# Kernel optimization log

Hardware: AMD Instinct MI355X
Metric: run time of the kernel (lower is better)

The kernel has to match this reference:

```python
import jax, jax.numpy as jnp
import numpy as np

H, C = 8, 16            # heads, per-head channels (at_channels)
HID = H * C             # 128
N_NODES = 50000
N_EDGES = 400000
N_GRAPHS = 500
SPEC = 1000


def setup_inputs() -> dict:
    key = jax.random.key(0)
    ks = jax.random.split(key, 32)
    s = 0.05

    def rn(k, shape):
        return jax.random.normal(k, shape, jnp.float32) * s

    inp = {}
    inp["x"] = jax.random.normal(ks[0], (N_NODES, 16), jnp.float32)
    inp["edge_index"] = jax.random.randint(ks[1], (2, N_EDGES), 0, N_NODES, jnp.int32)
    inp["edge_attr"] = jax.random.normal(ks[2], (N_EDGES, 2), jnp.float32)
    inp["batch"] = jnp.sort(jax.random.randint(ks[3], (N_NODES,), 0, N_GRAPHS, jnp.int32))
    # layer 1 (input dim 16)
    inp["at1_Wl"] = rn(ks[4], (16, HID)); inp["at1_bl"] = rn(ks[5], (HID,))
    inp["at1_Wr"] = rn(ks[6], (16, HID)); inp["at1_br"] = rn(ks[7], (HID,))
    inp["at1_We"] = rn(ks[8], (2, HID))
    inp["at1_att"] = rn(ks[9], (H, C))
    inp["at1_bias"] = rn(ks[10], (HID,))
    inp["l1_W"] = rn(ks[11], (16, HID)); inp["l1_b"] = rn(ks[12], (HID,))
    # layers 2..10 stacked (input dim 128)
    inp["atk_Wl"] = rn(ks[13], (9, HID, HID)); inp["atk_bl"] = rn(ks[14], (9, HID))
    inp["atk_Wr"] = rn(ks[15], (9, HID, HID)); inp["atk_br"] = rn(ks[16], (9, HID))
    inp["atk_We"] = rn(ks[17], (9, 2, HID))
    inp["atk_att"] = rn(ks[18], (9, H, C))
    inp["atk_bias"] = rn(ks[19], (9, HID))
    inp["lk_W"] = rn(ks[20], (9, HID, HID)); inp["lk_b"] = rn(ks[21], (9, HID))
    # readout
    inp["lin_W"] = rn(ks[22], (HID, SPEC)); inp["lin_b"] = rn(ks[23], (SPEC,))
    return inp


def _gatv2(x, src, dst, eattr, Wl, bl, Wr, br, We, att, bias):
    """PyG GATv2Conv forward (concat=True, slope=0.2, self-loops already in src/dst)."""
    N = x.shape[0]
    xl = (x @ Wl + bl).reshape(N, H, C)   # source transform
    xr = (x @ Wr + br).reshape(N, H, C)   # target transform
    ee = (eattr @ We).reshape(-1, H, C)   # edge embedding
    m = xl[src] + xr[dst] + ee            # [E, H, C]
    m = jnp.where(m > 0, m, 0.2 * m)      # leaky_relu
    logits = jnp.einsum('ehc,hc->eh', m, att)
    mx = jax.ops.segment_max(logits, dst, num_segments=N)
    ea = jnp.exp(logits - mx[dst])
    denom = jax.ops.segment_sum(ea, dst, num_segments=N)
    alpha = ea / jnp.maximum(denom[dst], 1e-16)
    out = jax.ops.segment_sum(xl[src] * alpha[:, :, None], dst, num_segments=N)
    return out.reshape(N, HID) + bias


def reference(x, edge_index, edge_attr, batch,
              at1_Wl, at1_bl, at1_Wr, at1_br, at1_We, at1_att, at1_bias, l1_W, l1_b,
              atk_Wl, atk_bl, atk_Wr, atk_br, atk_We, atk_att, atk_bias, lk_W, lk_b,
              lin_W, lin_b):
    N = x.shape[0]
    # add self loops once (edge_attr fill_value='mean', PyG default)
    sl = jnp.arange(N, dtype=edge_index.dtype)
    src = jnp.concatenate([edge_index[0], sl])
    dst = jnp.concatenate([edge_index[1], sl])
    ea = jnp.concatenate([edge_attr, jnp.broadcast_to(edge_attr.mean(0), (N, edge_attr.shape[1]))])

    h = jax.nn.elu(_gatv2(x, src, dst, ea, at1_Wl, at1_bl, at1_Wr, at1_br,
                          at1_We, at1_att, at1_bias) + x @ l1_W + l1_b)
    for i in range(9):  # layers 2..10
        h = jax.nn.elu(_gatv2(h, src, dst, ea, atk_Wl[i], atk_bl[i], atk_Wr[i], atk_br[i],
                              atk_We[i], atk_att[i], atk_bias[i]) + h @ lk_W[i] + lk_b[i])

    # global mean pool over graphs
    sums = jax.ops.segment_sum(h, batch, num_segments=N_GRAPHS)
    cnts = jax.ops.segment_sum(jnp.ones((N, 1), h.dtype), batch, num_segments=N_GRAPHS)
    g = sums / jnp.maximum(cnts, 1.0)
    return g @ lin_W + lin_b
```

## Files before the change

kernel.cpp:

```cpp
#include <hip/hip_runtime.h>
#include <hip/hip_bf16.h>
#include <cstdint>

#define HID 128

typedef __attribute__((ext_vector_type(8))) short bf16x8;
typedef __attribute__((ext_vector_type(4))) float f32x4;

__device__ __forceinline__ unsigned short f2bf(float x) {
    __hip_bfloat16 h = __float2bfloat16(x);
    return __builtin_bit_cast(unsigned short, h);
}
__device__ __forceinline__ float bf2f(unsigned short u) {
    return __bfloat162float(__builtin_bit_cast(__hip_bfloat16, u));
}
__device__ __forceinline__ float bflo(unsigned u) {
    return __builtin_bit_cast(float, u << 16);
}
__device__ __forceinline__ float bfhi(unsigned u) {
    return __builtin_bit_cast(float, u & 0xffff0000u);
}
__device__ __forceinline__ float4 ld4bf(const unsigned short* p) {
    ushort4 u = *(const ushort4*)p;
    return make_float4(bf2f(u.x), bf2f(u.y), bf2f(u.z), bf2f(u.w));
}
__device__ __forceinline__ int lower_bound_i(const int* a, int n, int v) {
    int lo = 0, hi = n;
    while (lo < hi) { int m = (lo + hi) >> 1; if (a[m] < v) lo = m + 1; else hi = m; }
    return lo;
}

__global__ __launch_bounds__(256) void mean_kernel(const float* __restrict__ eattr,
                                                   float* __restrict__ meansum, int E) {
    float sx = 0.f, sy = 0.f;
    for (int i = blockIdx.x * 256 + threadIdx.x; i < E; i += gridDim.x * 256) {
        float2 v = *(const float2*)(eattr + 2 * (size_t)i);
        sx += v.x; sy += v.y;
    }
    for (int d = 1; d < 64; d <<= 1) { sx += __shfl_xor(sx, d); sy += __shfl_xor(sy, d); }
    if ((threadIdx.x & 63) == 0) { atomicAdd(&meansum[0], sx); atomicAdd(&meansum[1], sy); }
}

__global__ __launch_bounds__(256) void deg_kernel(const int* __restrict__ ei,
                                                  int* __restrict__ deg, int E, int ET) {
    int e = blockIdx.x * 256 + threadIdx.x;
    if (e >= ET) return;
    int dst = (e < E) ? ei[E + e] : (e - E);
    atomicAdd(&deg[dst], 1);
}

__global__ __launch_bounds__(256) void scanA_kernel(const int* __restrict__ deg,
                                                    int* __restrict__ bsum, int N) {
    __shared__ int ws[4];
    int t = threadIdx.x;
    int base = blockIdx.x * 1024 + t * 4;
    int s = 0;
    #pragma unroll
    for (int j = 0; j < 4; j++) { int idx = base + j; if (idx < N) s += deg[idx]; }
    for (int d = 1; d < 64; d <<= 1) s += __shfl_xor(s, d);
    if ((t & 63) == 0) ws[t >> 6] = s;
    __syncthreads();
    if (t == 0) bsum[blockIdx.x] = ws[0] + ws[1] + ws[2] + ws[3];
}

__global__ __launch_bounds__(64) void scanB_kernel(const int* __restrict__ bsum,
                                                   int* __restrict__ boff,
                                                   int* __restrict__ row_ptr, int NB, int N) {
    int t = threadIdx.x;
    int v = (t < NB) ? bsum[t] : 0;
    int inc = v;
    #pragma unroll
    for (int d = 1; d < 64; d <<= 1) { int u = __shfl_up(inc, d); if (t >= d) inc += u; }
    if (t < NB) boff[t] = inc - v;
    if (t == 63) row_ptr[N] = inc;
}

__global__ __launch_bounds__(256) void scanC_kernel(const int* __restrict__ deg,
                                                    const int* __restrict__ boff,
                                                    int* __restrict__ row_ptr,
                                                    int* __restrict__ cursor, int N) {
    __shared__ int wsum[4];
    int t = threadIdx.x;
    int lane = t & 63, wid = t >> 6;
    int base = blockIdx.x * 1024 + t * 4;
    int v[4]; int s = 0;
    #pragma unroll
    for (int j = 0; j < 4; j++) { int idx = base + j; v[j] = (idx < N) ? deg[idx] : 0; s += v[j]; }
    int inc = s;
    #pragma unroll
    for (int d = 1; d < 64; d <<= 1) { int u = __shfl_up(inc, d); if (lane >= d) inc += u; }
    if (lane == 63) wsum[wid] = inc;
    __syncthreads();
    int woff = 0;
    for (int ww = 0; ww < wid; ww++) woff += wsum[ww];
    int excl = boff[blockIdx.x] + woff + inc - s;
    #pragma unroll
    for (int j = 0; j < 4; j++) {
        int idx = base + j;
        if (idx < N) { row_ptr[idx] = excl; cursor[idx] = excl; }
        excl += v[j];
    }
}

__global__ __launch_bounds__(256) void fill_kernel(const int* __restrict__ ei,
                                                   const float* __restrict__ eattr,
                                                   const float* __restrict__ meansum,
                                                   int* __restrict__ cursor,
                                                   int* __restrict__ csr_src,
                                                   unsigned int* __restrict__ csr_eap,
                                                   int E, int ET) {
    int e = blockIdx.x * 256 + threadIdx.x;
    if (e >= ET) return;
    int src, dst; float2 ea;
    if (e < E) {
        src = ei[e]; dst = ei[E + e];
        ea = *(const float2*)(eattr + 2 * (size_t)e);
    } else {
        src = dst = e - E;
        float inv = 1.0f / (float)E;
        ea.x = meansum[0] * inv; ea.y = meansum[1] * inv;
    }
    unsigned pea = (unsigned)f2bf(ea.x) | ((unsigned)f2bf(ea.y) << 16);
    int pos = atomicAdd(&cursor[dst], 1);
    csr_src[pos] = src;
    csr_eap[pos] = pea;
}

__global__ __launch_bounds__(256) void wprep_kernel(const float* __restrict__ src,
                                                    unsigned short* __restrict__ hi, int total) {
    int idx = blockIdx.x * 256 + threadIdx.x;
    if (idx >= total) return;
    int layer = idx >> 14;
    int rem = idx & 16383;
    int n = rem >> 7, k = rem & 127;
    hi[idx] = f2bf(src[(layer << 14) | (k << 7) | n]);
}

#define LROW 136
__global__ __launch_bounds__(256) void gemm3_kernel(
    const unsigned short* __restrict__ Hb,
    const unsigned short* __restrict__ W0h, const float* __restrict__ b0, unsigned short* __restrict__ o0,
    const unsigned short* __restrict__ W1h, const float* __restrict__ b1, unsigned short* __restrict__ o1,
    const unsigned short* __restrict__ W2h, const float* __restrict__ b2, unsigned short* __restrict__ o2,
    int N) {
    __shared__ unsigned short lds_h[128 * LROW];
    int y = blockIdx.y;
    const unsigned short* wsrc = (y == 0) ? W0h : (y == 1) ? W1h : W2h;
    const float* bias = (y == 0) ? b0 : (y == 1) ? b1 : b2;
    unsigned short* outp = (y == 0) ? o0 : (y == 1) ? o1 : o2;

    int tid = threadIdx.x;
    int wid = tid >> 6, lane = tid & 63;
    int row0 = blockIdx.x * 128 + wid * 32;
    int lr = lane & 15;
    int cgrp = lane >> 4;
    int kb = cgrp * 8;

    #pragma unroll
    for (int j = 0; j < 8; j++) {
        int c = tid + 256 * j;
        int r = c >> 4, col = (c & 15) * 8;
        *(bf16x8*)&lds_h[r * LROW + col] = *(const bf16x8*)(wsrc + r * HID + col);
    }

    bf16x8 ha[2][4];
    bool rowsok = (row0 < N);
    #pragma unroll
    for (int mf = 0; mf < 2; mf++) {
        int node = row0 + mf * 16 + lr;
        int nodec = (node < N) ? node : (N - 1);
        if (!rowsok) nodec = 0;
        const unsigned short* pa = Hb + (size_t)nodec * HID + kb;
        #pragma unroll
        for (int kf = 0; kf < 4; kf++) ha[mf][kf] = *(const bf16x8*)(pa + kf * 32);
    }

    __syncthreads();
    if (!rowsok) return;

    #pragma unroll 2
    for (int nf = 0; nf < 8; nf++) {
        int wrow = nf * 16 + lr;
        const unsigned short* ph = &lds_h[wrow * LROW + kb];
        bf16x8 wf[4];
        #pragma unroll
        for (int kf = 0; kf < 4; kf++) wf[kf] = *(const bf16x8*)(ph + kf * 32);
        f32x4 acc0 = {0.f, 0.f, 0.f, 0.f};
        f32x4 acc1 = {0.f, 0.f, 0.f, 0.f};
        #pragma unroll
        for (int kf = 0; kf < 4; kf++) {
            acc0 = __builtin_amdgcn_mfma_f32_16x16x32_bf16(wf[kf], ha[0][kf], acc0, 0, 0, 0);
            acc1 = __builtin_amdgcn_mfma_f32_16x16x32_bf16(wf[kf], ha[1][kf], acc1, 0, 0, 0);
        }
        int chb = nf * 16 + cgrp * 4;
        float4 bias4 = *(const float4*)(bias + chb);
        int node0 = row0 + lr;
        int node1 = row0 + 16 + lr;
        ushort4 u0, u1;
        u0.x = f2bf(acc0[0] + bias4.x); u0.y = f2bf(acc0[1] + bias4.y);
        u0.z = f2bf(acc0[2] + bias4.z); u0.w = f2bf(acc0[3] + bias4.w);
        u1.x = f2bf(acc1[0] + bias4.x); u1.y = f2bf(acc1[1] + bias4.y);
        u1.z = f2bf(acc1[2] + bias4.z); u1.w = f2bf(acc1[3] + bias4.w);
        if (node0 < N) *(ushort4*)(outp + (size_t)node0 * HID + chb) = u0;
        if (node1 < N) *(ushort4*)(outp + (size_t)node1 * HID + chb) = u1;
    }
}

__global__ __launch_bounds__(256) void transform16_kernel(
    const float* __restrict__ Hin,
    const float* __restrict__ W0, const float* __restrict__ b0, float* __restrict__ o0,
    const float* __restrict__ W1, const float* __restrict__ b1, float* __restrict__ o1,
    int N) {
    constexpr int K = 16;
    __shared__ float Ws[K][HID];
    __shared__ float Hs[32][K + 4];

    const float* W; const float* bias; float* outp;
    if (blockIdx.z == 0) { W = W0; bias = b0; outp = o0; }
    else                 { W = W1; bias = b1; outp = o1; }

    int row0 = blockIdx.x * 32;
    int tid = threadIdx.x;
    int tx = tid & 15, ty = tid >> 4;

    for (int i = tid; i < 32 * (K / 4); i += 256) {
        int r = i / (K / 4), kq = i % (K / 4);
        int row = row0 + r;
        float4 v = make_float4(0.f, 0.f, 0.f, 0.f);
        if (row < N) v = *(const float4*)(Hin + (size_t)row * K + kq * 4);
        *(float4*)&Hs[r][kq * 4] = v;
    }
    for (int i = tid; i < K * 32; i += 256) {
        int k = i >> 5, cq = i & 31;
        *(float4*)&Ws[k][cq * 4] = *(const float4*)(W + (size_t)k * HID + cq * 4);
    }
    __syncthreads();

    float acc[2][8];
    #pragma unroll
    for (int i = 0; i < 2; i++)
        #pragma unroll
        for (int j = 0; j < 8; j++) acc[i][j] = 0.f;

    int r0 = ty * 2, r1 = ty * 2 + 1;
    #pragma unroll
    for (int k = 0; k < K; k++) {
        float a0 = Hs[r0][k];
        float a1 = Hs[r1][k];
        float4 w0 = *(float4*)&Ws[k][tx * 4];
        float4 w1 = *(float4*)&Ws[k][64 + tx * 4];
        acc[0][0] += a0 * w0.x; acc[0][1] += a0 * w0.y; acc[0][2] += a0 * w0.z; acc[0][3] += a0 * w0.w;
        acc[0][4] += a0 * w1.x; acc[0][5] += a0 * w1.y; acc[0][6] += a0 * w1.z; acc[0][7] += a0 * w1.w;
        acc[1][0] += a1 * w0.x; acc[1][1] += a1 * w0.y; acc[1][2] += a1 * w0.z; acc[1][3] += a1 * w0.w;
        acc[1][4] += a1 * w1.x; acc[1][5] += a1 * w1.y; acc[1][6] += a1 * w1.z; acc[1][7] += a1 * w1.w;
    }

    float4 bb0 = *(const float4*)(bias + tx * 4);
    float4 bb1 = *(const float4*)(bias + 64 + tx * 4);
    #pragma unroll
    for (int i = 0; i < 2; i++) {
        int row = row0 + ty * 2 + i;
        if (row < N) {
            float4 v0 = make_float4(acc[i][0] + bb0.x, acc[i][1] + bb0.y, acc[i][2] + bb0.z, acc[i][3] + bb0.w);
            float4 v1 = make_float4(acc[i][4] + bb1.x, acc[i][5] + bb1.y, acc[i][6] + bb1.z, acc[i][7] + bb1.w);
            *(float4*)(outp + (size_t)row * HID + tx * 4) = v0;
            *(float4*)(outp + (size_t)row * HID + 64 + tx * 4) = v1;
        }
    }
}

__global__ __launch_bounds__(256) void combine16_kernel(
    const float* __restrict__ Hin,
    const float* __restrict__ W, const float* __restrict__ bias,
    const float* __restrict__ Att, unsigned short* __restrict__ Hb,
    int N) {
    constexpr int K = 16;
    __shared__ float Ws[K][HID];
    __shared__ float Hs[32][K + 4];

    int row0 = blockIdx.x * 32;
    int tid = threadIdx.x;
    int tx = tid & 15, ty = tid >> 4;

    for (int i = tid; i < 32 * (K / 4); i += 256) {
        int r = i / (K / 4), kq = i % (K / 4);
        int row = row0 + r;
        float4 v = make_float4(0.f, 0.f, 0.f, 0.f);
        if (row < N) v = *(const float4*)(Hin + (size_t)row * K + kq * 4);
        *(float4*)&Hs[r][kq * 4] = v;
    }
    for (int i = tid; i < K * 32; i += 256) {
        int k = i >> 5, cq = i & 31;
        *(float4*)&Ws[k][cq * 4] = *(const float4*)(W + (size_t)k * HID + cq * 4);
    }
    __syncthreads();

    float acc[2][8];
    #pragma unroll
    for (int i = 0; i < 2; i++)
        #pragma unroll
        for (int j = 0; j < 8; j++) acc[i][j] = 0.f;

    int r0 = ty * 2, r1 = ty * 2 + 1;
    #pragma unroll
    for (int k = 0; k < K; k++) {
        float a0 = Hs[r0][k];
        float a1 = Hs[r1][k];
        float4 w0 = *(float4*)&Ws[k][tx * 4];
        float4 w1 = *(float4*)&Ws[k][64 + tx * 4];
        acc[0][0] += a0 * w0.x; acc[0][1] += a0 * w0.y; acc[0][2] += a0 * w0.z; acc[0][3] += a0 * w0.w;
        acc[0][4] += a0 * w1.x; acc[0][5] += a0 * w1.y; acc[0][6] += a0 * w1.z; acc[0][7] += a0 * w1.w;
        acc[1][0] += a1 * w0.x; acc[1][1] += a1 * w0.y; acc[1][2] += a1 * w0.z; acc[1][3] += a1 * w0.w;
        acc[1][4] += a1 * w1.x; acc[1][5] += a1 * w1.y; acc[1][6] += a1 * w1.z; acc[1][7] += a1 * w1.w;
    }

    float4 bb0 = *(const float4*)(bias + tx * 4);
    float4 bb1 = *(const float4*)(bias + 64 + tx * 4);
    #pragma unroll
    for (int i = 0; i < 2; i++) {
        int row = row0 + ty * 2 + i;
        if (row < N) {
            const float* p0 = Att + (size_t)row * HID + tx * 4;
            float4 g0 = *(const float4*)p0;
            float4 g1 = *(const float4*)(p0 + 64);
            float v[8];
            v[0] = g0.x + acc[i][0] + bb0.x; v[1] = g0.y + acc[i][1] + bb0.y;
            v[2] = g0.z + acc[i][2] + bb0.z; v[3] = g0.w + acc[i][3] + bb0.w;
            v[4] = g1.x + acc[i][4] + bb1.x; v[5] = g1.y + acc[i][5] + bb1.y;
            v[6] = g1.z + acc[i][6] + bb1.z; v[7] = g1.w + acc[i][7] + bb1.w;
            #pragma unroll
            for (int j = 0; j < 8; j++) v[j] = (v[j] > 0.f) ? v[j] : (__expf(v[j]) - 1.f);
            ushort4 h0, h1;
            h0.x = f2bf(v[0]); h0.y = f2bf(v[1]); h0.z = f2bf(v[2]); h0.w = f2bf(v[3]);
            h1.x = f2bf(v[4]); h1.y = f2bf(v[5]); h1.z = f2bf(v[6]); h1.w = f2bf(v[7]);
            *(ushort4*)(Hb + (size_t)row * HID + tx * 4) = h0;
            *(ushort4*)(Hb + (size_t)row * HID + 64 + tx * 4) = h1;
        }
    }
}

template <int FUSE>
__global__ __launch_bounds__(256) void edge_kernel(
    const void* __restrict__ XLv, const void* __restrict__ XRv,
    const int* __restrict__ row_ptr, const int* __restrict__ csr_src,
    const unsigned int* __restrict__ csr_eap,
    const float* __restrict__ att,
    const float* __restrict__ We,
    const float* __restrict__ gbias,
    const unsigned short* __restrict__ lin,
    float* __restrict__ hf, unsigned short* __restrict__ hb,
    int N) {
    int n = (blockIdx.x * 256 + threadIdx.x) >> 6;
    int lane = threadIdx.x & 63;
    int half = lane >> 5;
    int l = lane & 31;
    bool active = (n < N);
    int nn = active ? n : 0;

    int c0 = l * 4;
    float4 av  = *(const float4*)(att + c0);
    float4 we0 = *(const float4*)(We + c0);
    float4 we1 = *(const float4*)(We + HID + c0);

    auto ldx = [&](const void* p, int idx) -> float4 {
        if constexpr (FUSE) return ld4bf((const unsigned short*)p + (size_t)idx * HID + c0);
        else                return *(const float4*)((const float*)p + (size_t)idx * HID + c0);
    };
    float4 xr = ldx(XRv, nn);

    int eb = 0, eend = 0;
    if (active) { eb = row_ptr[n]; eend = row_ptr[n + 1]; }
    int mid = (eb + eend + 1) >> 1;
    int sb = half ? mid : eb;
    int se = half ? eend : mid;

    float l_run = 0.f;
    float4 fa = make_float4(0.f, 0.f, 0.f, 0.f);

    for (int base = sb; base < se; base += 32) {
        int cnt = min(32, se - base);
        int myi = base + l;
        int msrc = 0; unsigned mea = 0;
        if (myi < se) { msrc = csr_src[myi]; mea = csr_eap[myi]; }

        int s0 = __shfl(msrc, 0, 32);
        int s1 = __shfl(msrc, 1, 32);
        unsigned e0 = __shfl(mea, 0, 32);
        unsigned e1 = __shfl(mea, 1, 32);
        float4 xl0 = ldx(XLv, s0);
        float4 xl1 = ldx(XLv, s1);

        for (int j = 0; ; j += 2) {
            bool more = (j + 2 < cnt);
            int ns0 = 0, ns1 = 0; unsigned ne0 = 0, ne1 = 0;
            float4 nxl0, nxl1;
            if (more) {
                ns0 = __shfl(msrc, j + 2, 32);
                ns1 = __shfl(msrc, j + 3, 32);
                ne0 = __shfl(mea, j + 2, 32);
                ne1 = __shfl(mea, j + 3, 32);
                nxl0 = ldx(XLv, ns0);
                nxl1 = ldx(XLv, ns1);
            }
            float ex0 = bflo(e0), ey0 = bfhi(e0);
            float ex1 = bflo(e1), ey1 = bfhi(e1);
            float t, part0, part1;
            float m0x = xl0.x + xr.x + ex0 * we0.x + ey0 * we1.x;
            float m0y = xl0.y + xr.y + ex0 * we0.y + ey0 * we1.y;
            float m0z = xl0.z + xr.z + ex0 * we0.z + ey0 * we1.z;
            float m0w = xl0.w + xr.w + ex0 * we0.w + ey0 * we1.w;
            m0x = fmaxf(m0x, 0.2f * m0x);
            m0y = fmaxf(m0y, 0.2f * m0y);
            m0z = fmaxf(m0z, 0.2f * m0z);
            m0w = fmaxf(m0w, 0.2f * m0w);
            part0 = m0x * av.x + m0y * av.y + m0z * av.z + m0w * av.w;
            float m1x = xl1.x + xr.x + ex1 * we0.x + ey1 * we1.x;
            float m1y = xl1.y + xr.y + ex1 * we0.y + ey1 * we1.y;
            float m1z = xl1.z + xr.z + ex1 * we0.z + ey1 * we1.z;
            float m1w = xl1.w + xr.w + ex1 * we0.w + ey1 * we1.w;
            m1x = fmaxf(m1x, 0.2f * m1x);
            m1y = fmaxf(m1y, 0.2f * m1y);
            m1z = fmaxf(m1z, 0.2f * m1z);
            m1w = fmaxf(m1w, 0.2f * m1w);
            part1 = m1x * av.x + m1y * av.y + m1z * av.z + m1w * av.w;
            t = __shfl_xor(part0, 1); part0 += t;
            t = __shfl_xor(part0, 2); part0 += t;
            t = __shfl_xor(part1, 1); part1 += t;
            t = __shfl_xor(part1, 2); part1 += t;

            bool two = (j + 1 < cnt);
            float p0 = __expf(fminf(part0, 60.f));
            float p1 = two ? __expf(fminf(part1, 60.f)) : 0.f;
            l_run += p0 + p1;
            fa.x += p0 * xl0.x + p1 * xl1.x;
            fa.y += p0 * xl0.y + p1 * xl1.y;
            fa.z += p0 * xl0.z + p1 * xl1.z;
            fa.w += p0 * xl0.w + p1 * xl1.w;
            if (!more) break;
            s0 = ns0; s1 = ns1; e0 = ne0; e1 = ne1; xl0 = nxl0; xl1 = nxl1;
        }
    }

    l_run += __shfl_xor(l_run, 32);
    fa.x += __shfl_xor(fa.x, 32);
    fa.y += __shfl_xor(fa.y, 32);
    fa.z += __shfl_xor(fa.z, 32);
    fa.w += __shfl_xor(fa.w, 32);

    if (!active || half) return;
    float inv = 1.f / fmaxf(l_run, 1e-16f);
    float4 bias4 = *(const float4*)(gbias + c0);
    float4 v;
    v.x = fa.x * inv + bias4.x;
    v.y = fa.y * inv + bias4.y;
    v.z = fa.z * inv + bias4.z;
    v.w = fa.w * inv + bias4.w;
    if constexpr (FUSE) {
        float4 lv = ld4bf(lin + (size_t)n * HID + c0);
        v.x += lv.x; v.y += lv.y; v.z += lv.z; v.w += lv.w;
        v.x = (v.x > 0.f) ? v.x : (__expf(v.x) - 1.f);
        v.y = (v.y > 0.f) ? v.y : (__expf(v.y) - 1.f);
        v.z = (v.z > 0.f) ? v.z : (__expf(v.z) - 1.f);
        v.w = (v.w > 0.f) ? v.w : (__expf(v.w) - 1.f);
        if (hf) *(float4*)(hf + (size_t)n * HID + c0) = v;
        ushort4 hh;
        hh.x = f2bf(v.x); hh.y = f2bf(v.y); hh.z = f2bf(v.z); hh.w = f2bf(v.w);
        *(ushort4*)(hb + (size_t)n * HID + c0) = hh;
    } else {
        *(float4*)(hf + (size_t)n * HID + c0) = v;
    }
}

__global__ __launch_bounds__(128) void pool_kernel(const float* __restrict__ h,
                                                   const int* __restrict__ batch,
                                                   float* __restrict__ g, int N) {
    int gid = blockIdx.x;
    int lo = lower_bound_i(batch, N, gid);
    int hi = lower_bound_i(batch, N, gid + 1);
    int c = threadIdx.x;
    float s = 0.f;
    for (int i = lo; i < hi; i++) s += h[(size_t)i * HID + c];
    g[gid * HID + c] = s / fmaxf((float)(hi - lo), 1.0f);
}

__global__ __launch_bounds__(256) void readout_kernel(const float* __restrict__ g,
                                                      const float* __restrict__ W,
                                                      const float* __restrict__ b,
                                                      float* __restrict__ out, int S) {
    __shared__ float gs[HID];
    int gid = blockIdx.y;
    if (threadIdx.x < HID) gs[threadIdx.x] = g[gid * HID + threadIdx.x];
    __syncthreads();
    int c = blockIdx.x * 256 + threadIdx.x;
    if (c < S) {
        float acc = b[c];
        #pragma unroll 8
        for (int k = 0; k < HID; k++) acc += gs[k] * W[(size_t)k * S + c];
        out[(size_t)gid * S + c] = acc;
    }
}

extern "C" void kernel_launch(void* const* d_in, const int* in_sizes, int n_in,
                              void* d_out, int out_size, void* d_ws, size_t ws_size,
                              hipStream_t stream) {
    const float* x      = (const float*)d_in[0];
    const int*   ei     = (const int*)d_in[1];
    const float* eattr  = (const float*)d_in[2];
    const int*   batch  = (const int*)d_in[3];
    const float* at1_Wl = (const float*)d_in[4];
    const float* at1_bl = (const float*)d_in[5];
    const float* at1_Wr = (const float*)d_in[6];
    const float* at1_br = (const float*)d_in[7];
    const float* at1_We = (const float*)d_in[8];
    const float* at1_att= (const float*)d_in[9];
    const float* at1_b  = (const float*)d_in[10];
    const float* l1_W   = (const float*)d_in[11];
    const float* l1_b   = (const float*)d_in[12];
    const float* atk_Wl = (const float*)d_in[13];
    const float* atk_bl = (const float*)d_in[14];
    const float* atk_Wr = (const float*)d_in[15];
    const float* atk_br = (const float*)d_in[16];
    const float* atk_We = (const float*)d_in[17];
    const float* atk_att= (const float*)d_in[18];
    const float* atk_b  = (const float*)d_in[19];
    const float* lk_W   = (const float*)d_in[20];
    const float* lk_b   = (const float*)d_in[21];
    const float* lin_W  = (const float*)d_in[22];
    const float* lin_b  = (const float*)d_in[23];
    float* out = (float*)d_out;

    const int N  = in_sizes[0] / 16;
    const int E  = in_sizes[1] / 2;
    const int ET = E + N;
    const int S  = 1000;
    const int G  = out_size / S;

    char* w = (char*)d_ws;
    auto alloc = [&](size_t bytes) -> char* {
        char* p = w; w += (bytes + 255) & ~(size_t)255; return p;
    };
    float*  XLf     = (float*)alloc((size_t)N * HID * 4);
    float*  XRf     = (float*)alloc((size_t)N * HID * 4);
    unsigned short* XLb = (unsigned short*)alloc((size_t)N * HID * 2);
    unsigned short* XRb = (unsigned short*)alloc((size_t)N * HID * 2);
    unsigned short* Linb = (unsigned short*)alloc((size_t)N * HID * 2);
    float*  Hf      = (float*)alloc((size_t)N * HID * 4);
    unsigned short* Hb = (unsigned short*)alloc((size_t)N * HID * 2);
    int*    deg     = (int*)alloc((size_t)N * 4);
    int*    row_ptr = (int*)alloc((size_t)(N + 1) * 4);
    int*    cursor  = (int*)alloc((size_t)N * 4);
    int*    csr_src = (int*)alloc((size_t)ET * 4);
    unsigned int* csr_eap = (unsigned int*)alloc((size_t)ET * 4);
    float*  meansum = (float*)alloc(8);
    int*    bsum    = (int*)alloc(256);
    int*    boff    = (int*)alloc(256);
    unsigned short* WlTh = (unsigned short*)alloc((size_t)9 * 16384 * 2);
    unsigned short* WrTh = (unsigned short*)alloc((size_t)9 * 16384 * 2);
    unsigned short* WkTh = (unsigned short*)alloc((size_t)9 * 16384 * 2);
    float*  gpool   = (float*)alloc((size_t)G * HID * 4);
    (void)ws_size; (void)n_in;

    hipMemsetAsync(deg, 0, (size_t)N * 4, stream);
    hipMemsetAsync(meansum, 0, 8, stream);

    const int wtot = 9 * 16384;
    wprep_kernel<<<(wtot + 255) / 256, 256, 0, stream>>>(atk_Wl, WlTh, wtot);
    wprep_kernel<<<(wtot + 255) / 256, 256, 0, stream>>>(atk_Wr, WrTh, wtot);
    wprep_kernel<<<(wtot + 255) / 256, 256, 0, stream>>>(lk_W,   WkTh, wtot);

    mean_kernel<<<256, 256, 0, stream>>>(eattr, meansum, E);
    deg_kernel<<<(ET + 255) / 256, 256, 0, stream>>>(ei, deg, E, ET);
    const int NB = (N + 1023) / 1024;
    scanA_kernel<<<NB, 256, 0, stream>>>(deg, bsum, N);
    scanB_kernel<<<1, 64, 0, stream>>>(bsum, boff, row_ptr, NB, N);
    scanC_kernel<<<NB, 256, 0, stream>>>(deg, boff, row_ptr, cursor, N);
    fill_kernel<<<(ET + 255) / 256, 256, 0, stream>>>(ei, eattr, meansum, cursor, csr_src, csr_eap, E, ET);

    const int gx16 = (N + 31) / 32;
    const int ge   = (N + 3) / 4;
    const int gx3  = (N + 127) / 128;

    transform16_kernel<<<dim3(gx16, 1, 2), 256, 0, stream>>>(x, at1_Wl, at1_bl, XLf, at1_Wr, at1_br, XRf, N);
    edge_kernel<0><<<ge, 256, 0, stream>>>(XLf, XRf, row_ptr, csr_src, csr_eap, at1_att, at1_We, at1_b,
                                           nullptr, Hf, nullptr, N);
    combine16_kernel<<<gx16, 256, 0, stream>>>(x, l1_W, l1_b, Hf, Hb, N);

    for (int i = 0; i < 9; i++) {
        const unsigned short* wlh = WlTh + (size_t)i * 16384;
        const unsigned short* wrh = WrTh + (size_t)i * 16384;
        const unsigned short* wkh = WkTh + (size_t)i * 16384;
        const float* bl = atk_bl + (size_t)i * HID;
        const float* br = atk_br + (size_t)i * HID;
        const float* bk = lk_b   + (size_t)i * HID;
        const float* Wep = atk_We + (size_t)i * 2 * HID;
        const float* at = atk_att + (size_t)i * HID;
        const float* ab = atk_b  + (size_t)i * HID;

        gemm3_kernel<<<dim3(gx3, 3), 256, 0, stream>>>(Hb,
                                                       wlh, bl, XLb,
                                                       wrh, br, XRb,
                                                       wkh, bk, Linb, N);
        edge_kernel<1><<<ge, 256, 0, stream>>>(XLb, XRb, row_ptr, csr_src, csr_eap, at, Wep, ab,
                                               Linb, (i == 8) ? Hf : nullptr, Hb, N);
    }

    pool_kernel<<<G, 128, 0, stream>>>(Hf, batch, gpool, N);
    readout_kernel<<<dim3((S + 255) / 256, G), 256, 0, stream>>>(gpool, lin_W, lin_b, out, S);
}
```

Measured before the change: 771.3 us.

## Reuse activation tile across three GEMMs and split edge aggregation four ways

The gemm3 kernel now loads each 64-row activation tile once into registers and loops over the three weight matrices. It restages each weight matrix in LDS between barriers, where before one grid dimension was launched per weight and each block read the activations again. Separately, the edge kernel splits each node's edge list across four 16-lane quarters with 8 channels per lane, replacing two 32-lane halves with 4 channels per lane. This gives more edge-level parallelism per node and wider 16-byte gathers, at the cost of an extra cross-lane reduction stage and more registers per lane.

```diff
diff --git a/kernel.cpp b/kernel.cpp
--- a/kernel.cpp
+++ b/kernel.cpp
@@ -5,6 +5,7 @@
 #define HID 128
 
 typedef __attribute__((ext_vector_type(8))) short bf16x8;
+typedef __attribute__((ext_vector_type(8))) unsigned short u16x8;
 typedef __attribute__((ext_vector_type(4))) float f32x4;
 
 __device__ __forceinline__ unsigned short f2bf(float x) {
@@ -144,65 +145,60 @@
     const unsigned short* __restrict__ W2h, const float* __restrict__ b2, unsigned short* __restrict__ o2,
     int N) {
     __shared__ unsigned short lds_h[128 * LROW];
-    int y = blockIdx.y;
-    const unsigned short* wsrc = (y == 0) ? W0h : (y == 1) ? W1h : W2h;
-    const float* bias = (y == 0) ? b0 : (y == 1) ? b1 : b2;
-    unsigned short* outp = (y == 0) ? o0 : (y == 1) ? o1 : o2;
-
     int tid = threadIdx.x;
     int wid = tid >> 6, lane = tid & 63;
-    int row0 = blockIdx.x * 128 + wid * 32;
+    int row0 = blockIdx.x * 64 + wid * 16;
     int lr = lane & 15;
     int cgrp = lane >> 4;
     int kb = cgrp * 8;
-
-    #pragma unroll
-    for (int j = 0; j < 8; j++) {
-        int c = tid + 256 * j;
-        int r = c >> 4, col = (c & 15) * 8;
-        *(bf16x8*)&lds_h[r * LROW + col] = *(const bf16x8*)(wsrc + r * HID + col);
-    }
-
-    bf16x8 ha[2][4];
     bool rowsok = (row0 < N);
-    #pragma unroll
-    for (int mf = 0; mf < 2; mf++) {
-        int node = row0 + mf * 16 + lr;
-        int nodec = (node < N) ? node : (N - 1);
-        if (!rowsok) nodec = 0;
+
+    bf16x8 ha[4];
+    {
+        int node = row0 + lr;
+        int nodec = rowsok ? ((node < N) ? node : (N - 1)) : 0;
         const unsigned short* pa = Hb + (size_t)nodec * HID + kb;
         #pragma unroll
-        for (int kf = 0; kf < 4; kf++) ha[mf][kf] = *(const bf16x8*)(pa + kf * 32);
-    }
-
-    __syncthreads();
-    if (!rowsok) return;
-
-    #pragma unroll 2
-    for (int nf = 0; nf < 8; nf++) {
-        int wrow = nf * 16 + lr;
-        const unsigned short* ph = &lds_h[wrow * LROW + kb];
-        bf16x8 wf[4];
+        for (int kf = 0; kf < 4; kf++) ha[kf] = *(const bf16x8*)(pa + kf * 32);
+    }
+
+    const unsigned short* Whs[3] = {W0h, W1h, W2h};
+    const float* Bs[3] = {b0, b1, b2};
+    unsigned short* Os[3] = {o0, o1, o2};
+
+    for (int w = 0; w < 3; w++) {
+        if (w) __syncthreads();
+        const unsigned short* sh = Whs[w];
         #pragma unroll
-        for (int kf = 0; kf < 4; kf++) wf[kf] = *(const bf16x8*)(ph + kf * 32);
-        f32x4 acc0 = {0.f, 0.f, 0.f, 0.f};
-        f32x4 acc1 = {0.f, 0.f, 0.f, 0.f};
-        #pragma unroll
-        for (int kf = 0; kf < 4; kf++) {
-            acc0 = __builtin_amdgcn_mfma_f32_16x16x32_bf16(wf[kf], ha[0][kf], acc0, 0, 0, 0);
-            acc1 = __builtin_amdgcn_mfma_f32_16x16x32_bf16(wf[kf], ha[1][kf], acc1, 0, 0, 0);
+        for (int j = 0; j < 8; j++) {
+            int c = tid + 256 * j;
+            int r = c >> 4, col = (c & 15) * 8;
+            *(bf16x8*)&lds_h[r * LROW + col] = *(const bf16x8*)(sh + r * HID + col);
         }
-        int chb = nf * 16 + cgrp * 4;
-        float4 bias4 = *(const float4*)(bias + chb);
-        int node0 = row0 + lr;
-        int node1 = row0 + 16 + lr;
-        ushort4 u0, u1;
-        u0.x = f2bf(acc0[0] + bias4.x); u0.y = f2bf(acc0[1] + bias4.y);
-        u0.z = f2bf(acc0[2] + bias4.z); u0.w = f2bf(acc0[3] + bias4.w);
-        u1.x = f2bf(acc1[0] + bias4.x); u1.y = f2bf(acc1[1] + bias4.y);
-        u1.z = f2bf(acc1[2] + bias4.z); u1.w = f2bf(acc1[3] + bias4.w);
-        if (node0 < N) *(ushort4*)(outp + (size_t)node0 * HID + chb) = u0;
-        if (node1 < N) *(ushort4*)(outp + (size_t)node1 * HID + chb) = u1;
+        __syncthreads();
+        if (!rowsok) continue;
+
+        const float* bias = Bs[w];
+        unsigned short* outp = Os[w];
+        #pragma unroll 2
+        for (int nf = 0; nf < 8; nf++) {
+            int wrow = nf * 16 + lr;
+            const unsigned short* ph = &lds_h[wrow * LROW + kb];
+            bf16x8 wf[4];
+            #pragma unroll
+            for (int kf = 0; kf < 4; kf++) wf[kf] = *(const bf16x8*)(ph + kf * 32);
+            f32x4 acc = {0.f, 0.f, 0.f, 0.f};
+            #pragma unroll
+            for (int kf = 0; kf < 4; kf++)
+                acc = __builtin_amdgcn_mfma_f32_16x16x32_bf16(wf[kf], ha[kf], acc, 0, 0, 0);
+            int chb = nf * 16 + cgrp * 4;
+            float4 bias4 = *(const float4*)(bias + chb);
+            int node = row0 + lr;
+            ushort4 u;
+            u.x = f2bf(acc[0] + bias4.x); u.y = f2bf(acc[1] + bias4.y);
+            u.z = f2bf(acc[2] + bias4.z); u.w = f2bf(acc[3] + bias4.w);
+            if (node < N) *(ushort4*)(outp + (size_t)node * HID + chb) = u;
+        }
     }
 }
 
@@ -340,6 +336,32 @@
 }
 
 template <int FUSE>
+__device__ __forceinline__ void ldx8(const void* p, int idx, int c0, float4& a, float4& b) {
+    if constexpr (FUSE) {
+        u16x8 u = *(const u16x8*)((const unsigned short*)p + (size_t)idx * HID + c0);
+        a = make_float4(bf2f(u[0]), bf2f(u[1]), bf2f(u[2]), bf2f(u[3]));
+        b = make_float4(bf2f(u[4]), bf2f(u[5]), bf2f(u[6]), bf2f(u[7]));
+    } else {
+        const float* f = (const float*)p + (size_t)idx * HID + c0;
+        a = *(const float4*)f;
+        b = *(const float4*)(f + 4);
+    }
+}
+
+__device__ __forceinline__ float logit4(float4 xl, float4 xr, float ex, float ey,
+                                        float4 w0, float4 w1, float4 av) {
+    float mx = xl.x + xr.x + ex * w0.x + ey * w1.x;
+    float my = xl.y + xr.y + ex * w0.y + ey * w1.y;
+    float mz = xl.z + xr.z + ex * w0.z + ey * w1.z;
+    float mw = xl.w + xr.w + ex * w0.w + ey * w1.w;
+    mx = fmaxf(mx, 0.2f * mx);
+    my = fmaxf(my, 0.2f * my);
+    mz = fmaxf(mz, 0.2f * mz);
+    mw = fmaxf(mw, 0.2f * mw);
+    return mx * av.x + my * av.y + mz * av.z + mw * av.w;
+}
+
+template <int FUSE>
 __global__ __launch_bounds__(256) void edge_kernel(
     const void* __restrict__ XLv, const void* __restrict__ XRv,
     const int* __restrict__ row_ptr, const int* __restrict__ csr_src,
@@ -352,122 +374,128 @@
     int N) {
     int n = (blockIdx.x * 256 + threadIdx.x) >> 6;
     int lane = threadIdx.x & 63;
-    int half = lane >> 5;
-    int l = lane & 31;
+    int q = lane >> 4;
+    int l = lane & 15;
     bool active = (n < N);
     int nn = active ? n : 0;
 
-    int c0 = l * 4;
-    float4 av  = *(const float4*)(att + c0);
-    float4 we0 = *(const float4*)(We + c0);
-    float4 we1 = *(const float4*)(We + HID + c0);
-
-    auto ldx = [&](const void* p, int idx) -> float4 {
-        if constexpr (FUSE) return ld4bf((const unsigned short*)p + (size_t)idx * HID + c0);
-        else                return *(const float4*)((const float*)p + (size_t)idx * HID + c0);
-    };
-    float4 xr = ldx(XRv, nn);
+    int c0 = l * 8;
+    float4 av0 = *(const float4*)(att + c0),       av1 = *(const float4*)(att + c0 + 4);
+    float4 w00 = *(const float4*)(We + c0),        w01 = *(const float4*)(We + c0 + 4);
+    float4 w10 = *(const float4*)(We + HID + c0),  w11 = *(const float4*)(We + HID + c0 + 4);
+
+    float4 xr0, xr1;
+    ldx8<FUSE>(XRv, nn, c0, xr0, xr1);
 
     int eb = 0, eend = 0;
     if (active) { eb = row_ptr[n]; eend = row_ptr[n + 1]; }
-    int mid = (eb + eend + 1) >> 1;
-    int sb = half ? mid : eb;
-    int se = half ? eend : mid;
+    int len = eend - eb;
+    int qs = eb + ((len * q) >> 2);
+    int qe = eb + ((len * (q + 1)) >> 2);
 
     float l_run = 0.f;
-    float4 fa = make_float4(0.f, 0.f, 0.f, 0.f);
-
-    for (int base = sb; base < se; base += 32) {
-        int cnt = min(32, se - base);
+    float4 fa0 = make_float4(0.f, 0.f, 0.f, 0.f);
+    float4 fa1 = make_float4(0.f, 0.f, 0.f, 0.f);
+
+    for (int base = qs; base < qe; base += 16) {
+        int cnt = min(16, qe - base);
         int myi = base + l;
         int msrc = 0; unsigned mea = 0;
-        if (myi < se) { msrc = csr_src[myi]; mea = csr_eap[myi]; }
-
-        int s0 = __shfl(msrc, 0, 32);
-        int s1 = __shfl(msrc, 1, 32);
-        unsigned e0 = __shfl(mea, 0, 32);
-        unsigned e1 = __shfl(mea, 1, 32);
-        float4 xl0 = ldx(XLv, s0);
-        float4 xl1 = ldx(XLv, s1);
+        if (myi < qe) { msrc = csr_src[myi]; mea = csr_eap[myi]; }
+
+        int s0 = __shfl(msrc, 0, 16);
+        int s1 = __shfl(msrc, 1, 16);
+        unsigned e0 = __shfl(mea, 0, 16);
+        unsigned e1 = __shfl(mea, 1, 16);
+        float4 xl0a, xl0b, xl1a, xl1b;
+        ldx8<FUSE>(XLv, s0, c0, xl0a, xl0b);
+        ldx8<FUSE>(XLv, s1, c0, xl1a, xl1b);
 
         for (int j = 0; ; j += 2) {
             bool more = (j + 2 < cnt);
             int ns0 = 0, ns1 = 0; unsigned ne0 = 0, ne1 = 0;
-            float4 nxl0, nxl1;
+            float4 nxl0a, nxl0b, nxl1a, nxl1b;
             if (more) {
-                ns0 = __shfl(msrc, j + 2, 32);
-                ns1 = __shfl(msrc, j + 3, 32);
-                ne0 = __shfl(mea, j + 2, 32);
-                ne1 = __shfl(mea, j + 3, 32);
-                nxl0 = ldx(XLv, ns0);
-                nxl1 = ldx(XLv, ns1);
+                ns0 = __shfl(msrc, j + 2, 16);
+                ns1 = __shfl(msrc, j + 3, 16);
+                ne0 = __shfl(mea, j + 2, 16);
+                ne1 = __shfl(mea, j + 3, 16);
+                ldx8<FUSE>(XLv, ns0, c0, nxl0a, nxl0b);
+                ldx8<FUSE>(XLv, ns1, c0, nxl1a, nxl1b);
             }
             float ex0 = bflo(e0), ey0 = bfhi(e0);
             float ex1 = bflo(e1), ey1 = bfhi(e1);
-            float t, part0, part1;
-            float m0x = xl0.x + xr.x + ex0 * we0.x + ey0 * we1.x;
-            float m0y = xl0.y + xr.y + ex0 * we0.y + ey0 * we1.y;
-            float m0z = xl0.z + xr.z + ex0 * we0.z + ey0 * we1.z;
-            float m0w = xl0.w + xr.w + ex0 * we0.w + ey0 * we1.w;
-            m0x = fmaxf(m0x, 0.2f * m0x);
-            m0y = fmaxf(m0y, 0.2f * m0y);
-            m0z = fmaxf(m0z, 0.2f * m0z);
-            m0w = fmaxf(m0w, 0.2f * m0w);
-            part0 = m0x * av.x + m0y * av.y + m0z * av.z + m0w * av.w;
-            float m1x = xl1.x + xr.x + ex1 * we0.x + ey1 * we1.x;
-            float m1y = xl1.y + xr.y + ex1 * we0.y + ey1 * we1.y;
-            float m1z = xl1.z + xr.z + ex1 * we0.z + ey1 * we1.z;
-            float m1w = xl1.w + xr.w + ex1 * we0.w + ey1 * we1.w;
-            m1x = fmaxf(m1x, 0.2f * m1x);
-            m1y = fmaxf(m1y, 0.2f * m1y);
-            m1z = fmaxf(m1z, 0.2f * m1z);
-            m1w = fmaxf(m1w, 0.2f * m1w);
-            part1 = m1x * av.x + m1y * av.y + m1z * av.z + m1w * av.w;
-            t = __shfl_xor(part0, 1); part0 += t;
-            t = __shfl_xor(part0, 2); part0 += t;
-            t = __shfl_xor(part1, 1); part1 += t;
-            t = __shfl_xor(part1, 2); part1 += t;
+            float part0 = logit4(xl0a, xr0, ex0, ey0, w00, w10, av0)
+                        + logit4(xl0b, xr1, ex0, ey0, w01, w11, av1);
+            float part1 = logit4(xl1a, xr0, ex1, ey1, w00, w10, av0)
+                        + logit4(xl1b, xr1, ex1, ey1, w01, w11, av1);
+            part0 += __shfl_xor(part0, 1);
+            part1 += __shfl_xor(part1, 1);
 
             bool two = (j + 1 < cnt);
             float p0 = __expf(fminf(part0, 60.f));
             float p1 = two ? __expf(fminf(part1, 60.f)) : 0.f;
             l_run += p0 + p1;
-            fa.x += p0 * xl0.x + p1 * xl1.x;
-            fa.y += p0 * xl0.y + p1 * xl1.y;
-            fa.z += p0 * xl0.z + p1 * xl1.z;
-            fa.w += p0 * xl0.w + p1 * xl1.w;
+            fa0.x += p0 * xl0a.x + p1 * xl1a.x;
+            fa0.y += p0 * xl0a.y + p1 * xl1a.y;
+            fa0.z += p0 * xl0a.z + p1 * xl1a.z;
+            fa0.w += p0 * xl0a.w + p1 * xl1a.w;
+            fa1.x += p0 * xl0b.x + p1 * xl1b.x;
+            fa1.y += p0 * xl0b.y + p1 * xl1b.y;
+            fa1.z += p0 * xl0b.z + p1 * xl1b.z;
+            fa1.w += p0 * xl0b.w + p1 * xl1b.w;
             if (!more) break;
-            s0 = ns0; s1 = ns1; e0 = ne0; e1 = ne1; xl0 = nxl0; xl1 = nxl1;
+            s0 = ns0; s1 = ns1; e0 = ne0; e1 = ne1;
+            xl0a = nxl0a; xl0b = nxl0b; xl1a = nxl1a; xl1b = nxl1b;
         }
     }
 
-    l_run += __shfl_xor(l_run, 32);
-    fa.x += __shfl_xor(fa.x, 32);
-    fa.y += __shfl_xor(fa.y, 32);
-    fa.z += __shfl_xor(fa.z, 32);
-    fa.w += __shfl_xor(fa.w, 32);
-
-    if (!active || half) return;
+    #pragma unroll
+    for (int d = 16; d <= 32; d <<= 1) {
+        l_run += __shfl_xor(l_run, d);
+        fa0.x += __shfl_xor(fa0.x, d);
+        fa0.y += __shfl_xor(fa0.y, d);
+        fa0.z += __shfl_xor(fa0.z, d);
+        fa0.w += __shfl_xor(fa0.w, d);
+        fa1.x += __shfl_xor(fa1.x, d);
+        fa1.y += __shfl_xor(fa1.y, d);
+        fa1.z += __shfl_xor(fa1.z, d);
+        fa1.w += __shfl_xor(fa1.w, d);
+    }
+
+    if (!active || q != 0) return;
     float inv = 1.f / fmaxf(l_run, 1e-16f);
-    float4 bias4 = *(const float4*)(gbias + c0);
-    float4 v;
-    v.x = fa.x * inv + bias4.x;
-    v.y = fa.y * inv + bias4.y;
-    v.z = fa.z * inv + bias4.z;
-    v.w = fa.w * inv + bias4.w;
+    float4 b0 = *(const float4*)(gbias + c0);
+    float4 b1 = *(const float4*)(gbias + c0 + 4);
+    float4 v0, v1;
+    v0.x = fa0.x * inv + b0.x; v0.y = fa0.y * inv + b0.y;
+    v0.z = fa0.z * inv + b0.z; v0.w = fa0.w * inv + b0.w;
+    v1.x = fa1.x * inv + b1.x; v1.y = fa1.y * inv + b1.y;
+    v1.z = fa1.z * inv + b1.z; v1.w = fa1.w * inv + b1.w;
     if constexpr (FUSE) {
-        float4 lv = ld4bf(lin + (size_t)n * HID + c0);
-        v.x += lv.x; v.y += lv.y; v.z += lv.z; v.w += lv.w;
-        v.x = (v.x > 0.f) ? v.x : (__expf(v.x) - 1.f);
-        v.y = (v.y > 0.f) ? v.y : (__expf(v.y) - 1.f);
-        v.z = (v.z > 0.f) ? v.z : (__expf(v.z) - 1.f);
-        v.w = (v.w > 0.f) ? v.w : (__expf(v.w) - 1.f);
-        if (hf) *(float4*)(hf + (size_t)n * HID + c0) = v;
-        ushort4 hh;
-        hh.x = f2bf(v.x); hh.y = f2bf(v.y); hh.z = f2bf(v.z); hh.w = f2bf(v.w);
-        *(ushort4*)(hb + (size_t)n * HID + c0) = hh;
+        float4 lv0, lv1;
+        ldx8<1>(lin, n, c0, lv0, lv1);
+        v0.x += lv0.x; v0.y += lv0.y; v0.z += lv0.z; v0.w += lv0.w;
+        v1.x += lv1.x; v1.y += lv1.y; v1.z += lv1.z; v1.w += lv1.w;
+        v0.x = (v0.x > 0.f) ? v0.x : (__expf(v0.x) - 1.f);
+        v0.y = (v0.y > 0.f) ? v0.y : (__expf(v0.y) - 1.f);
+        v0.z = (v0.z > 0.f) ? v0.z : (__expf(v0.z) - 1.f);
+        v0.w = (v0.w > 0.f) ? v0.w : (__expf(v0.w) - 1.f);
+        v1.x = (v1.x > 0.f) ? v1.x : (__expf(v1.x) - 1.f);
+        v1.y = (v1.y > 0.f) ? v1.y : (__expf(v1.y) - 1.f);
+        v1.z = (v1.z > 0.f) ? v1.z : (__expf(v1.z) - 1.f);
+        v1.w = (v1.w > 0.f) ? v1.w : (__expf(v1.w) - 1.f);
+        if (hf) {
+            *(float4*)(hf + (size_t)n * HID + c0) = v0;
+            *(float4*)(hf + (size_t)n * HID + c0 + 4) = v1;
+        }
+        u16x8 hh;
+        hh[0] = f2bf(v0.x); hh[1] = f2bf(v0.y); hh[2] = f2bf(v0.z); hh[3] = f2bf(v0.w);
+        hh[4] = f2bf(v1.x); hh[5] = f2bf(v1.y); hh[6] = f2bf(v1.z); hh[7] = f2bf(v1.w);
+        *(u16x8*)(hb + (size_t)n * HID + c0) = hh;
     } else {
-        *(float4*)(hf + (size_t)n * HID + c0) = v;
+        *(float4*)(hf + (size_t)n * HID + c0) = v0;
+        *(float4*)(hf + (size_t)n * HID + c0 + 4) = v1;
     }
 }
 
@@ -578,7 +606,7 @@
 
     const int gx16 = (N + 31) / 32;
     const int ge   = (N + 3) / 4;
-    const int gx3  = (N + 127) / 128;
+    const int gx3  = (N + 63) / 64;
 
     transform16_kernel<<<dim3(gx16, 1, 2), 256, 0, stream>>>(x, at1_Wl, at1_bl, XLf, at1_Wr, at1_br, XRf, N);
     edge_kernel<0><<<ge, 256, 0, stream>>>(XLf, XRf, row_ptr, csr_src, csr_eap, at1_att, at1_We, at1_b,
@@ -596,10 +624,10 @@
         const float* at = atk_att + (size_t)i * HID;
         const float* ab = atk_b  + (size_t)i * HID;
 
-        gemm3_kernel<<<dim3(gx3, 3), 256, 0, stream>>>(Hb,
-                                                       wlh, bl, XLb,
-                                                       wrh, br, XRb,
-                                                       wkh, bk, Linb, N);
+        gemm3_kernel<<<gx3, 256, 0, stream>>>(Hb,
+                                              wlh, bl, XLb,
+                                              wrh, br, XRb,
+                                              wkh, bk, Linb, N);
         edge_kernel<1><<<ge, 256, 0, stream>>>(XLb, XRb, row_ptr, csr_src, csr_eap, at, Wep, ab,
                                                Linb, (i == 8) ? Hf : nullptr, Hb, N);
     }
```

Measured after the change: 884.5 us. 14.7% more time.

## Reuse loaded activation rows across all three weight matrices in gemm3

Applied to the files above, without the earlier changes.

The three-output GEMM previously launched a grid dimension per weight matrix, so every block reloaded the same activation rows from global memory three times. Now each block loads 64 activation rows once into registers and loops over the three weight matrices, restaging each into LDS with barriers in between. This cuts activation traffic by a factor of three. In exchange, each block performs three serialized weight loads, handles fewer rows per wave, and must synchronize between matrices.

```diff
diff --git a/kernel.cpp b/kernel.cpp
--- a/kernel.cpp
+++ b/kernel.cpp
@@ -144,65 +144,60 @@
     const unsigned short* __restrict__ W2h, const float* __restrict__ b2, unsigned short* __restrict__ o2,
     int N) {
     __shared__ unsigned short lds_h[128 * LROW];
-    int y = blockIdx.y;
-    const unsigned short* wsrc = (y == 0) ? W0h : (y == 1) ? W1h : W2h;
-    const float* bias = (y == 0) ? b0 : (y == 1) ? b1 : b2;
-    unsigned short* outp = (y == 0) ? o0 : (y == 1) ? o1 : o2;
-
     int tid = threadIdx.x;
     int wid = tid >> 6, lane = tid & 63;
-    int row0 = blockIdx.x * 128 + wid * 32;
+    int row0 = blockIdx.x * 64 + wid * 16;
     int lr = lane & 15;
     int cgrp = lane >> 4;
     int kb = cgrp * 8;
-
-    #pragma unroll
-    for (int j = 0; j < 8; j++) {
-        int c = tid + 256 * j;
-        int r = c >> 4, col = (c & 15) * 8;
-        *(bf16x8*)&lds_h[r * LROW + col] = *(const bf16x8*)(wsrc + r * HID + col);
-    }
-
-    bf16x8 ha[2][4];
     bool rowsok = (row0 < N);
-    #pragma unroll
-    for (int mf = 0; mf < 2; mf++) {
-        int node = row0 + mf * 16 + lr;
-        int nodec = (node < N) ? node : (N - 1);
-        if (!rowsok) nodec = 0;
+
+    bf16x8 ha[4];
+    {
+        int node = row0 + lr;
+        int nodec = rowsok ? ((node < N) ? node : (N - 1)) : 0;
         const unsigned short* pa = Hb + (size_t)nodec * HID + kb;
         #pragma unroll
-        for (int kf = 0; kf < 4; kf++) ha[mf][kf] = *(const bf16x8*)(pa + kf * 32);
-    }
-
-    __syncthreads();
-    if (!rowsok) return;
-
-    #pragma unroll 2
-    for (int nf = 0; nf < 8; nf++) {
-        int wrow = nf * 16 + lr;
-        const unsigned short* ph = &lds_h[wrow * LROW + kb];
-        bf16x8 wf[4];
+        for (int kf = 0; kf < 4; kf++) ha[kf] = *(const bf16x8*)(pa + kf * 32);
+    }
+
+    const unsigned short* Whs[3] = {W0h, W1h, W2h};
+    const float* Bs[3] = {b0, b1, b2};
+    unsigned short* Os[3] = {o0, o1, o2};
+
+    for (int w = 0; w < 3; w++) {
+        if (w) __syncthreads();
+        const unsigned short* sh = Whs[w];
         #pragma unroll
-        for (int kf = 0; kf < 4; kf++) wf[kf] = *(const bf16x8*)(ph + kf * 32);
-        f32x4 acc0 = {0.f, 0.f, 0.f, 0.f};
-        f32x4 acc1 = {0.f, 0.f, 0.f, 0.f};
-        #pragma unroll
-        for (int kf = 0; kf < 4; kf++) {
-            acc0 = __builtin_amdgcn_mfma_f32_16x16x32_bf16(wf[kf], ha[0][kf], acc0, 0, 0, 0);
-            acc1 = __builtin_amdgcn_mfma_f32_16x16x32_bf16(wf[kf], ha[1][kf], acc1, 0, 0, 0);
+        for (int j = 0; j < 8; j++) {
+            int c = tid + 256 * j;
+            int r = c >> 4, col = (c & 15) * 8;
+            *(bf16x8*)&lds_h[r * LROW + col] = *(const bf16x8*)(sh + r * HID + col);
         }
-        int chb = nf * 16 + cgrp * 4;
-        float4 bias4 = *(const float4*)(bias + chb);
-        int node0 = row0 + lr;
-        int node1 = row0 + 16 + lr;
-        ushort4 u0, u1;
-        u0.x = f2bf(acc0[0] + bias4.x); u0.y = f2bf(acc0[1] + bias4.y);
-        u0.z = f2bf(acc0[2] + bias4.z); u0.w = f2bf(acc0[3] + bias4.w);
-        u1.x = f2bf(acc1[0] + bias4.x); u1.y = f2bf(acc1[1] + bias4.y);
-        u1.z = f2bf(acc1[2] + bias4.z); u1.w = f2bf(acc1[3] + bias4.w);
-        if (node0 < N) *(ushort4*)(outp + (size_t)node0 * HID + chb) = u0;
-        if (node1 < N) *(ushort4*)(outp + (size_t)node1 * HID + chb) = u1;
+        __syncthreads();
+        if (!rowsok) continue;
+
+        const float* bias = Bs[w];
+        unsigned short* outp = Os[w];
+        #pragma unroll 2
+        for (int nf = 0; nf < 8; nf++) {
+            int wrow = nf * 16 + lr;
+            const unsigned short* ph = &lds_h[wrow * LROW + kb];
+            bf16x8 wf[4];
+            #pragma unroll
+            for (int kf = 0; kf < 4; kf++) wf[kf] = *(const bf16x8*)(ph + kf * 32);
+            f32x4 acc = {0.f, 0.f, 0.f, 0.f};
+            #pragma unroll
+            for (int kf = 0; kf < 4; kf++)
+                acc = __builtin_amdgcn_mfma_f32_16x16x32_bf16(wf[kf], ha[kf], acc, 0, 0, 0);
+            int chb = nf * 16 + cgrp * 4;
+            float4 bias4 = *(const float4*)(bias + chb);
+            int node = row0 + lr;
+            ushort4 u;
+            u.x = f2bf(acc[0] + bias4.x); u.y = f2bf(acc[1] + bias4.y);
+            u.z = f2bf(acc[2] + bias4.z); u.w = f2bf(acc[3] + bias4.w);
+            if (node < N) *(ushort4*)(outp + (size_t)node * HID + chb) = u;
+        }
     }
 }
 
@@ -578,7 +573,7 @@
 
     const int gx16 = (N + 31) / 32;
     const int ge   = (N + 3) / 4;
-    const int gx3  = (N + 127) / 128;
+    const int gx3  = (N + 63) / 64;
 
     transform16_kernel<<<dim3(gx16, 1, 2), 256, 0, stream>>>(x, at1_Wl, at1_bl, XLf, at1_Wr, at1_br, XRf, N);
     edge_kernel<0><<<ge, 256, 0, stream>>>(XLf, XRf, row_ptr, csr_src, csr_eap, at1_att, at1_We, at1_b,
@@ -596,10 +591,10 @@
         const float* at = atk_att + (size_t)i * HID;
         const float* ab = atk_b  + (size_t)i * HID;
 
-        gemm3_kernel<<<dim3(gx3, 3), 256, 0, stream>>>(Hb,
-                                                       wlh, bl, XLb,
-                                                       wrh, br, XRb,
-                                                       wkh, bk, Linb, N);
+        gemm3_kernel<<<gx3, 256, 0, stream>>>(Hb,
+                                              wlh, bl, XLb,
+                                              wrh, br, XRb,
+                                              wkh, bk, Linb, N);
         edge_kernel<1><<<ge, 256, 0, stream>>>(XLb, XRb, row_ptr, csr_src, csr_eap, at, Wep, ab,
                                                Linb, (i == 8) ? Hf : nullptr, Hb, N);
     }
```

New measurement: 754.9 us. 1.02x faster.
